# Kernel optimization log

Hardware: AMD Instinct MI355X
Metric: run time of the kernel (lower is better)

The kernel has to match this reference:

```python
import jax, jax.numpy as jnp
import numpy as np

N = 100000
F_IN = 256
F_HID = 256
F_OUT = 40
E = 3200000


def setup_inputs() -> dict:
    key = jax.random.key(0)
    ks = jax.random.split(key, 8)
    x = jax.random.normal(ks[0], (N, F_IN), dtype=jnp.float32)
    edge_index = jax.random.randint(ks[1], (2, E), 0, N, dtype=jnp.int64)
    s1 = 1.0 / np.sqrt(F_IN)
    s2 = 1.0 / np.sqrt(F_HID)
    W1 = jax.random.uniform(ks[2], (F_IN, F_HID), jnp.float32, -s1, s1)
    b1 = jnp.zeros((F_HID,), jnp.float32)
    W2 = jax.random.uniform(ks[3], (F_HID, F_HID), jnp.float32, -s2, s2)
    b2 = jnp.zeros((F_HID,), jnp.float32)
    Wlin = jax.random.uniform(ks[4], (F_HID, F_OUT), jnp.float32, -s2, s2)
    blin = jax.random.uniform(ks[5], (F_OUT,), jnp.float32, -s2, s2)
    return {"x": x, "edge_index": edge_index, "W1": W1, "b1": b1,
            "W2": W2, "b2": b2, "Wlin": Wlin, "blin": blin}


def _gcn_conv(x, src, dst, deg_inv_sqrt, W, b):
    # PyG GCNConv: linear transform, then sym-normalized aggregation, then bias
    h = x @ W                                    # [N, F]
    coef = deg_inv_sqrt[src] * deg_inv_sqrt[dst]  # [E+N]
    msgs = h[src] * coef[:, None]                # gather + scale
    agg = jax.ops.segment_sum(msgs, dst, num_segments=x.shape[0])
    return agg + b


def reference(x, edge_index, W1, b1, W2, b2, Wlin, blin):
    n = x.shape[0]
    # add self-loops (static shape: E + N)
    loops = jnp.arange(n, dtype=edge_index.dtype)
    src = jnp.concatenate([edge_index[0], loops])
    dst = jnp.concatenate([edge_index[1], loops])
    deg = jax.ops.segment_sum(jnp.ones_like(dst, dtype=x.dtype), dst, num_segments=n)
    deg_inv_sqrt = jnp.where(deg > 0, jax.lax.rsqrt(deg), 0.0)
    # dropout is identity in eval mode (training=False)
    h = _gcn_conv(x, src, dst, deg_inv_sqrt, W1, b1)
    h = _gcn_conv(h, src, dst, deg_inv_sqrt, W2, b2)
    logits = h @ Wlin + blin
    return jax.nn.log_softmax(logits, axis=1)
```

## Files before the change

kernel.cpp:

```cpp
#include <hip/hip_runtime.h>
#include <hip/hip_bf16.h>

#define FDIM 256
#define FOUT 40
#define RPB 256

typedef __attribute__((ext_vector_type(8))) short short8;
typedef __attribute__((ext_vector_type(4))) float floatx4;

__device__ __forceinline__ float bf2f(unsigned short u) {
  unsigned int x = ((unsigned int)u) << 16;
  float f;
  __builtin_memcpy(&f, &x, 4);
  return f;
}
__device__ __forceinline__ unsigned short f2bf(float f) {
  __hip_bfloat16 h = __float2bfloat16(f);
  unsigned short u;
  __builtin_memcpy(&u, &h, 2);
  return u;
}
__device__ __forceinline__ float blo(unsigned int v) {
  unsigned int x = v << 16; float f; __builtin_memcpy(&f, &x, 4); return f;
}
__device__ __forceinline__ float bhi(unsigned int v) {
  unsigned int x = v & 0xFFFF0000u; float f; __builtin_memcpy(&f, &x, 4); return f;
}


__global__ void detect_k(const int* __restrict__ raw, int nwords, int* __restrict__ flag) {
  if (threadIdx.x == 0) *flag = 0;
  __syncthreads();
  int found = 0;
  for (int w = 1 + 2 * threadIdx.x; w < nwords; w += 512)
    if (raw[w] != 0) { found = 1; break; }
  if (found) atomicOr(flag, 1);
}

__global__ void normalize_k(const int* __restrict__ raw, const int* __restrict__ flag,
                            int* __restrict__ srcN, int* __restrict__ dstN, int e) {
  int i = blockIdx.x * 256 + threadIdx.x;
  if (i >= e) return;
  if (*flag) {
    srcN[i] = raw[i];
    dstN[i] = raw[e + i];
  } else {
    srcN[i] = raw[2 * i];
    dstN[i] = raw[2 * (e + i)];
  }
}


__global__ void zero_cnt_k(int* cnt, int n) {
  int i = blockIdx.x * 256 + threadIdx.x;
  if (i < n) cnt[i] = 0;
}

__global__ void count_k(const int* __restrict__ dst, int* __restrict__ cnt, int e, int n) {
  int i = blockIdx.x * 256 + threadIdx.x;
  if (i < e) {
    int d = dst[i];
    if (d >= 0 && d < n) atomicAdd(&cnt[d], 1);
  }
}

__global__ void dis_leg_k(const int* __restrict__ cnt, float* __restrict__ dis, int n) {
  int i = blockIdx.x * 256 + threadIdx.x;
  if (i < n) dis[i] = rsqrtf((float)cnt[i] + 1.0f);
}

__global__ void scan_a_k(const int* __restrict__ cnt, int* __restrict__ excl,
                         int* __restrict__ bsum, int n) {
  __shared__ int sh[1024];
  int t = threadIdx.x;
  int gid = blockIdx.x * 1024 + t;
  int v = (gid < n) ? cnt[gid] : 0;
  sh[t] = v;
  __syncthreads();
  for (int off = 1; off < 1024; off <<= 1) {
    int x = (t >= off) ? sh[t - off] : 0;
    __syncthreads();
    sh[t] += x;
    __syncthreads();
  }
  if (gid < n) excl[gid] = sh[t] - v;
  if (t == 1023) bsum[blockIdx.x] = sh[1023];
}

__global__ void scan_b_k(int* __restrict__ bsum, int nb) {
  __shared__ int sh[1024];
  int t = threadIdx.x;
  int v = (t < nb) ? bsum[t] : 0;
  sh[t] = v;
  __syncthreads();
  for (int off = 1; off < 1024; off <<= 1) {
    int x = (t >= off) ? sh[t - off] : 0;
    __syncthreads();
    sh[t] += x;
    __syncthreads();
  }
  if (t < nb) bsum[t] = sh[t] - v;
}

__global__ void scan_c_k(int* __restrict__ row_ptr, const int* __restrict__ bsum,
                         const int* __restrict__ cnt, int* __restrict__ cursor, int n) {
  int gid = blockIdx.x * 1024 + threadIdx.x;
  if (gid < n) {
    int r = row_ptr[gid] + bsum[blockIdx.x];
    row_ptr[gid] = r;
    cursor[gid] = r;
    if (gid == n - 1) row_ptr[n] = r + cnt[gid];
  }
}

__global__ void fill_k(const int* __restrict__ src, const int* __restrict__ dst,
                       int* __restrict__ cursor, int* __restrict__ col, int e, int n) {
  int i = blockIdx.x * 256 + threadIdx.x;
  if (i < e) {
    int d = dst[i];
    if (d >= 0 && d < n) {
      int slot = atomicAdd(&cursor[d], 1);
      int s = src[i];
      s = min(max(s, 0), n - 1);
      col[slot] = s;
    }
  }
}


__global__ __launch_bounds__(512) void zerob_k(int* __restrict__ bcnt, int nbuck) {
  int t = threadIdx.x;
  if (t < nbuck) bcnt[t] = 0;
}

__global__ __launch_bounds__(256) void bhist_k(
    const int* __restrict__ raw, const int* __restrict__ flag,
    int* __restrict__ bcnt, int e, int n, int nbuck, int cpb) {
  __shared__ int hist[512];
  int t = threadIdx.x;
  for (int b = t; b < nbuck; b += 256) hist[b] = 0;
  __syncthreads();
  int fl = *flag;
  int start = blockIdx.x * cpb;
  int endc = min(e, start + cpb);
  for (int i = start + t; i < endc; i += 256) {
    int d = fl ? raw[e + i] : raw[2 * (e + i)];
    if (d >= 0 && d < n) atomicAdd(&hist[d >> 8], 1);
  }
  __syncthreads();
  for (int b = t; b < nbuck; b += 256)
    if (hist[b]) atomicAdd(&bcnt[b], hist[b]);
}

__global__ __launch_bounds__(512) void bscan_k(
    const int* __restrict__ bcnt, int* __restrict__ bbase,
    int* __restrict__ bcur, int nbuck) {
  __shared__ int sh[512];
  int t = threadIdx.x;
  int v = (t < nbuck) ? bcnt[t] : 0;
  sh[t] = v;
  __syncthreads();
  for (int off = 1; off < 512; off <<= 1) {
    int x = (t >= off) ? sh[t - off] : 0;
    __syncthreads();
    sh[t] += x;
    __syncthreads();
  }
  if (t < nbuck) {
    int ex = sh[t] - v;
    bbase[t] = ex;
    bcur[t] = ex;
  }
  if (t == nbuck - 1) bbase[nbuck] = sh[t];
}

__global__ __launch_bounds__(1024) void bin2_k(
    const int* __restrict__ raw, const int* __restrict__ flag,
    int* __restrict__ bcur, unsigned int* __restrict__ binned,
    int e, int n, int nbuck, int cpb) {
  __shared__ int hist[512];
  __shared__ int base_[512];
  __shared__ int cnt2[512];
  int t = threadIdx.x;
  int fl = *flag;
  int start = blockIdx.x * cpb;
  int endc = min(e, start + cpb);
  for (int b = t; b < nbuck; b += 1024) { hist[b] = 0; cnt2[b] = 0; }
  __syncthreads();
  for (int i = start + t; i < endc; i += 1024) {
    int d = fl ? raw[e + i] : raw[2 * (e + i)];
    if (d >= 0 && d < n) atomicAdd(&hist[d >> 8], 1);
  }
  __syncthreads();
  for (int b = t; b < nbuck; b += 1024) {
    int h = hist[b];
    base_[b] = h ? atomicAdd(&bcur[b], h) : 0;
  }
  __syncthreads();
  for (int i = start + t; i < endc; i += 1024) {
    int d = fl ? raw[e + i] : raw[2 * (e + i)];
    if (d >= 0 && d < n) {
      int s = fl ? raw[i] : raw[2 * i];
      s = min(max(s, 0), n - 1);
      int bk = d >> 8;
      int pos = base_[bk] + atomicAdd(&cnt2[bk], 1);
      binned[pos] = (((unsigned int)(d & 255)) << 17) | (unsigned int)s;
    }
  }
}

__global__ __launch_bounds__(256) void scatcnt_k(
    const unsigned int* __restrict__ binned, const int* __restrict__ bbase,
    int* __restrict__ row_ptr, float* __restrict__ dis,
    int* __restrict__ col, int n) {
  __shared__ int cnt[RPB];
  __shared__ int sc[RPB];
  __shared__ int cur[RPB];
  int b = blockIdx.x;
  int r0 = b * RPB;
  int r1 = min(n, r0 + RPB);
  int nr = r1 - r0;
  int t = threadIdx.x;
  cnt[t] = 0;
  __syncthreads();
  int e0 = bbase[b], e1 = bbase[b + 1];
  for (int i = e0 + t; i < e1; i += 256)
    atomicAdd(&cnt[binned[i] >> 17], 1);
  __syncthreads();
  int v = cnt[t];
  if (t < nr) dis[r0 + t] = rsqrtf((float)v + 1.0f);
  sc[t] = v;
  __syncthreads();
  for (int off = 1; off < 256; off <<= 1) {
    int x = (t >= off) ? sc[t - off] : 0;
    __syncthreads();
    sc[t] += x;
    __syncthreads();
  }
  int base = e0 + sc[t] - v;
  cur[t] = base;
  if (t < nr) row_ptr[r0 + t] = base;
  if (t == 0 && r1 == n) row_ptr[n] = e1;
  __syncthreads();
  for (int i = e0 + t; i < e1; i += 256) {
    unsigned int p = binned[i];
    int dlow = (int)(p >> 17);
    int slot = atomicAdd(&cur[dlow], 1);
    col[slot] = (int)(p & 0x1FFFF);
  }
}


__global__ __launch_bounds__(64) void wc_k(const float* __restrict__ W2,
                                           const float* __restrict__ Wlin,
                                           float* __restrict__ Wc) {
  __shared__ float row[FDIM];
  int k = blockIdx.x, t = threadIdx.x;
  for (int j = t; j < FDIM; j += 64) row[j] = W2[(size_t)k * FDIM + j];
  __syncthreads();
  if (t < FOUT) {
    float acc = 0.f;
    for (int j = 0; j < FDIM; ++j) acc += row[j] * Wlin[(size_t)j * FOUT + t];
    Wc[(size_t)k * FOUT + t] = acc;
  }
}

__global__ __launch_bounds__(64) void wfull_k(const float* __restrict__ W1,
                                              const float* __restrict__ Wc,
                                              float* __restrict__ Wfull) {
  __shared__ float row[FDIM];
  int k = blockIdx.x, t = threadIdx.x;
  for (int j = t; j < FDIM; j += 64) row[j] = W1[(size_t)k * FDIM + j];
  __syncthreads();
  if (t < FOUT) {
    float acc = 0.f;
    for (int j = 0; j < FDIM; ++j) acc += row[j] * Wc[(size_t)j * FOUT + t];
    Wfull[(size_t)k * FOUT + t] = acc;
  }
}

__global__ __launch_bounds__(64) void rvec_k(const float* __restrict__ b1,
                                             const float* __restrict__ Wc,
                                             const float* __restrict__ b2,
                                             const float* __restrict__ Wlin,
                                             const float* __restrict__ blin,
                                             float* __restrict__ b1c,
                                             float* __restrict__ r2) {
  int t = threadIdx.x;
  if (t < FOUT) {
    float a = 0.f, b = blin[t];
    for (int j = 0; j < FDIM; ++j) {
      a += b1[j] * Wc[(size_t)j * FOUT + t];
      b += b2[j] * Wlin[(size_t)j * FOUT + t];
    }
    b1c[t] = a;
    r2[t] = b;
  }
}

__global__ void wft_k(const float* __restrict__ Wfull, unsigned short* __restrict__ WfT) {
  int o = blockIdx.x, k = threadIdx.x;
  WfT[(size_t)o * FDIM + k] = (o < FOUT) ? f2bf(Wfull[(size_t)k * FOUT + o]) : (unsigned short)0;
}


__global__ __launch_bounds__(256) void proj_k(
    const float* __restrict__ X, const unsigned short* __restrict__ WfT,
    const float* __restrict__ dis, unsigned int* __restrict__ Ys32, int M) {
  __shared__ __align__(16) unsigned short Asm[64 * 40];
  __shared__ __align__(16) unsigned short Bsm[48 * 264];
  int t = threadIdx.x;
  int block_m = blockIdx.x * 64;
  int lane = t & 63, wave = t >> 6;
  int q = lane >> 4, rcol = lane & 15;
  for (int idx = t; idx < 48 * 256; idx += 256) {
    int o = idx >> 8, k = idx & 255;
    Bsm[o * 264 + k] = WfT[(size_t)o * FDIM + k];
  }
  floatx4 acc[3] = {};
  int arow = t >> 2, cc = (t & 3) * 8;
  int gm = block_m + arow;
  for (int kk = 0; kk < FDIM; kk += 32) {
    __syncthreads();
    {
      float4 v0 = {0, 0, 0, 0}, v1 = {0, 0, 0, 0};
      if (gm < M) {
        v0 = *(const float4*)(X + (size_t)gm * FDIM + kk + cc);
        v1 = *(const float4*)(X + (size_t)gm * FDIM + kk + cc + 4);
      }
      short8 pk;
      pk[0] = (short)f2bf(v0.x); pk[1] = (short)f2bf(v0.y);
      pk[2] = (short)f2bf(v0.z); pk[3] = (short)f2bf(v0.w);
      pk[4] = (short)f2bf(v1.x); pk[5] = (short)f2bf(v1.y);
      pk[6] = (short)f2bf(v1.z); pk[7] = (short)f2bf(v1.w);
      *(short8*)(Asm + arow * 40 + cc) = pk;
    }
    __syncthreads();
    short8 af = *(const short8*)(Asm + (wave * 16 + rcol) * 40 + q * 8);
    short8 b0 = *(const short8*)(Bsm + (rcol)*264 + kk + q * 8);
    short8 b1f = *(const short8*)(Bsm + (16 + rcol) * 264 + kk + q * 8);
    short8 b2f = *(const short8*)(Bsm + (32 + rcol) * 264 + kk + q * 8);
    acc[0] = __builtin_amdgcn_mfma_f32_16x16x32_bf16(af, b0, acc[0], 0, 0, 0);
    acc[1] = __builtin_amdgcn_mfma_f32_16x16x32_bf16(af, b1f, acc[1], 0, 0, 0);
    acc[2] = __builtin_amdgcn_mfma_f32_16x16x32_bf16(af, b2f, acc[2], 0, 0, 0);
  }
  __syncthreads();
#pragma unroll
  for (int rr = 0; rr < 4; ++rr) {
    int ml = wave * 16 + q * 4 + rr;
    int m = block_m + ml;
    float sc = (m < M) ? dis[m] : 0.f;
    unsigned short* lrow = Asm + ml * 40;
    lrow[rcol] = f2bf(acc[0][rr] * sc);
    lrow[16 + rcol] = f2bf(acc[1][rr] * sc);
    if (rcol < 8) lrow[32 + rcol] = f2bf(acc[2][rr] * sc);
  }
  __syncthreads();
  const unsigned int* A32 = (const unsigned int*)Asm;
  for (int idx = t; idx < 64 * 20; idx += 256) {
    int r = idx / 20, c = idx - r * 20;
    int m = block_m + r;
    if (m < M) Ys32[(size_t)m * 20 + c] = A32[idx];
  }
}


__global__ __launch_bounds__(256) void agg1_k(
    const unsigned int* __restrict__ T32, const int* __restrict__ row_ptr,
    const int* __restrict__ col, const float* __restrict__ dis,
    const float* __restrict__ b1c, unsigned int* __restrict__ O32, int n) {
  int wave = threadIdx.x >> 6, lane = threadIdx.x & 63;
  int wid = blockIdx.x * 4 + wave;
  int nw = gridDim.x * 4;
  int e = lane / 20;
  int fp = lane - e * 20;
  if (e > 2) { e = 2; fp = 19; }
  bool e0 = (e == 0), e1 = (e == 1);
  bool g0 = e0;
  float2 bv = ((const float2*)b1c)[fp];
  for (int i = wid; i < n; i += nw) {
    unsigned int sv = T32[(size_t)i * 20 + fp];
    float a0 = g0 ? blo(sv) : 0.f;
    float a1 = g0 ? bhi(sv) : 0.f;
    int beg = row_ptr[i], end = row_ptr[i + 1];
    for (int j0 = beg; j0 < end; j0 += 64) {
      int jj = j0 + lane;
      int cs = (jj < end) ? col[jj] : 0;
      int cc = min(64, end - j0);
      int kf = cc - cc % 24;
      int k = 0;
      for (; k < kf; k += 24) {
        int sel[8];
#pragma unroll
        for (int u = 0; u < 8; ++u) {
          int sa = __builtin_amdgcn_readlane(cs, k + 3 * u);
          int sb = __builtin_amdgcn_readlane(cs, k + 3 * u + 1);
          int sc2 = __builtin_amdgcn_readlane(cs, k + 3 * u + 2);
          sel[u] = e0 ? sa : (e1 ? sb : sc2);
        }
        unsigned int g[8];
#pragma unroll
        for (int u = 0; u < 8; ++u) g[u] = T32[(size_t)sel[u] * 20 + fp];
#pragma unroll
        for (int u = 0; u < 8; ++u) { a0 += blo(g[u]); a1 += bhi(g[u]); }
      }
      if (k < cc) {
        int sel[8];
        float w[8];
#pragma unroll
        for (int u = 0; u < 8; ++u) {
          int kb = k + 3 * u;
          int sa = __builtin_amdgcn_readlane(cs, kb & 63);
          int sb = __builtin_amdgcn_readlane(cs, (kb + 1) & 63);
          int sc2 = __builtin_amdgcn_readlane(cs, (kb + 2) & 63);
          sel[u] = e0 ? sa : (e1 ? sb : sc2);
          w[u] = (kb + e < cc) ? 1.f : 0.f;
        }
        unsigned int g[8];
#pragma unroll
        for (int u = 0; u < 8; ++u) g[u] = T32[(size_t)sel[u] * 20 + fp];
#pragma unroll
        for (int u = 0; u < 8; ++u) {
          a0 = fmaf(w[u], blo(g[u]), a0);
          a1 = fmaf(w[u], bhi(g[u]), a1);
        }
      }
    }
    a0 += __shfl(a0, fp + 20) + __shfl(a0, fp + 40);
    a1 += __shfl(a1, fp + 20) + __shfl(a1, fp + 40);
    if (g0) {
      float di = dis[i];
      unsigned int p = (unsigned int)f2bf((di * a0 + bv.x) * di) |
                       ((unsigned int)f2bf((di * a1 + bv.y) * di) << 16);
      O32[(size_t)i * 20 + fp] = p;
    }
  }
}

__global__ __launch_bounds__(256) void agg2_k(
    const unsigned int* __restrict__ T32, const int* __restrict__ row_ptr,
    const int* __restrict__ col, const float* __restrict__ dis,
    const float* __restrict__ r2, float* __restrict__ out, int n) {
  int wave = threadIdx.x >> 6, lane = threadIdx.x & 63;
  int wid = blockIdx.x * 4 + wave;
  int nw = gridDim.x * 4;
  int e = lane / 20;
  int fp = lane - e * 20;
  if (e > 2) { e = 2; fp = 19; }
  bool e0 = (e == 0), e1 = (e == 1);
  bool g0 = e0;
  float2 rv = ((const float2*)r2)[fp];
  for (int i = wid; i < n; i += nw) {
    unsigned int sv = T32[(size_t)i * 20 + fp];
    float a0 = g0 ? blo(sv) : 0.f;
    float a1 = g0 ? bhi(sv) : 0.f;
    int beg = row_ptr[i], end = row_ptr[i + 1];
    for (int j0 = beg; j0 < end; j0 += 64) {
      int jj = j0 + lane;
      int cs = (jj < end) ? col[jj] : 0;
      int cc = min(64, end - j0);
      int kf = cc - cc % 24;
      int k = 0;
      for (; k < kf; k += 24) {
        int sel[8];
#pragma unroll
        for (int u = 0; u < 8; ++u) {
          int sa = __builtin_amdgcn_readlane(cs, k + 3 * u);
          int sb = __builtin_amdgcn_readlane(cs, k + 3 * u + 1);
          int sc2 = __builtin_amdgcn_readlane(cs, k + 3 * u + 2);
          sel[u] = e0 ? sa : (e1 ? sb : sc2);
        }
        unsigned int g[8];
#pragma unroll
        for (int u = 0; u < 8; ++u) g[u] = T32[(size_t)sel[u] * 20 + fp];
#pragma unroll
        for (int u = 0; u < 8; ++u) { a0 += blo(g[u]); a1 += bhi(g[u]); }
      }
      if (k < cc) {
        int sel[8];
        float w[8];
#pragma unroll
        for (int u = 0; u < 8; ++u) {
          int kb = k + 3 * u;
          int sa = __builtin_amdgcn_readlane(cs, kb & 63);
          int sb = __builtin_amdgcn_readlane(cs, (kb + 1) & 63);
          int sc2 = __builtin_amdgcn_readlane(cs, (kb + 2) & 63);
          sel[u] = e0 ? sa : (e1 ? sb : sc2);
          w[u] = (kb + e < cc) ? 1.f : 0.f;
        }
        unsigned int g[8];
#pragma unroll
        for (int u = 0; u < 8; ++u) g[u] = T32[(size_t)sel[u] * 20 + fp];
#pragma unroll
        for (int u = 0; u < 8; ++u) {
          a0 = fmaf(w[u], blo(g[u]), a0);
          a1 = fmaf(w[u], bhi(g[u]), a1);
        }
      }
    }
    a0 += __shfl(a0, fp + 20) + __shfl(a0, fp + 40);
    a1 += __shfl(a1, fp + 20) + __shfl(a1, fp + 40);
    float di = dis[i];
    float v0 = g0 ? (di * a0 + rv.x) : -3.4e38f;
    float v1 = g0 ? (di * a1 + rv.y) : -3.4e38f;
    float m = fmaxf(v0, v1);
#pragma unroll
    for (int off = 32; off; off >>= 1) m = fmaxf(m, __shfl_xor(m, off));
    float s = g0 ? (__expf(v0 - m) + __expf(v1 - m)) : 0.f;
#pragma unroll
    for (int off = 32; off; off >>= 1) s += __shfl_xor(s, off);
    float lg = m + __logf(s);
    if (g0) {
      float2 o = {v0 - lg, v1 - lg};
      *(float2*)(out + (size_t)i * FOUT + 2 * fp) = o;
    }
  }
}


extern "C" void kernel_launch(void* const* d_in, const int* in_sizes, int n_in,
                              void* d_out, int out_size, void* d_ws, size_t ws_size,
                              hipStream_t stream) {
  const float* x   = (const float*)d_in[0];
  const int* eraw  = (const int*)d_in[1];
  const float* W1  = (const float*)d_in[2];
  const float* b1  = (const float*)d_in[3];
  const float* W2  = (const float*)d_in[4];
  const float* b2  = (const float*)d_in[5];
  const float* Wl  = (const float*)d_in[6];
  const float* bl  = (const float*)d_in[7];
  float* out = (float*)d_out;

  const int N = in_sizes[0] / FDIM;
  const int E = in_sizes[1] / 2;

  char* w = (char*)d_ws;
  size_t off = 0;
  auto take = [&](size_t bytes) {
    void* p = w + off;
    off = (off + bytes + 255) & ~(size_t)255;
    return p;
  };
  int* cnt     = (int*)take((size_t)N * 4);
  int* cursor  = (int*)take((size_t)N * 4);
  int* row_ptr = (int*)take((size_t)(N + 1) * 4);
  float* dis   = (float*)take((size_t)N * 4);
  int* bsum    = (int*)take(4096);
  int* eflag   = (int*)take(256);
  int* bcnt    = (int*)take(512 * 4);
  int* bbase   = (int*)take(513 * 4);
  int* bcur    = (int*)take(512 * 4);
  float* Wc    = (float*)take((size_t)FDIM * FOUT * 4);
  float* Wfull = (float*)take((size_t)FDIM * FOUT * 4);
  unsigned short* WfT = (unsigned short*)take((size_t)48 * FDIM * 2);
  float* b1c   = (float*)take(256);
  float* r2    = (float*)take(256);
  int* colx    = (int*)take((size_t)E * 4);

  size_t pairBytes = (size_t)2 * E * 4;
  size_t tabBytes  = (size_t)N * FOUT * 2;
  size_t rABytes = pairBytes > tabBytes ? pairBytes : tabBytes;
  char* regionA = (char*)take(rABytes);
  int* srcN = (int*)regionA;
  int* dstN = srcN + E;
  unsigned int* Ys32 = (unsigned int*)regionA;
  size_t binBytes = (size_t)E * 4;
  size_t rBBytes = binBytes > tabBytes ? binBytes : tabBytes;
  char* regionB = (char*)take(rBBytes);
  unsigned int* binned = (unsigned int*)regionB;
  unsigned int* Z1s32 = (unsigned int*)regionB;
  (void)n_in; (void)out_size; (void)ws_size;

  int gE = (E + 255) / 256;
  int gN = (N + 255) / 256;
  int NB = (N + 1023) / 1024;
  int gP = (N + 63) / 64;
  int nbuck = (N + RPB - 1) / RPB;
  bool bucketed = (N <= (1 << 17));

  int probe_words = 65536 < 2 * E ? 65536 : 2 * E;
  hipLaunchKernelGGL(detect_k, dim3(1), dim3(256), 0, stream, eraw, probe_words, eflag);

  if (bucketed) {
    int nblk = 256;
    int cpb = (E + nblk - 1) / nblk;
    hipLaunchKernelGGL(zerob_k, dim3(1), dim3(512), 0, stream, bcnt, nbuck);
    hipLaunchKernelGGL(bhist_k, dim3(nblk), dim3(256), 0, stream,
                       eraw, eflag, bcnt, E, N, nbuck, cpb);
    hipLaunchKernelGGL(bscan_k, dim3(1), dim3(512), 0, stream, bcnt, bbase, bcur, nbuck);
    hipLaunchKernelGGL(bin2_k, dim3(nblk), dim3(1024), 0, stream,
                       eraw, eflag, bcur, binned, E, N, nbuck, cpb);
    hipLaunchKernelGGL(scatcnt_k, dim3(nbuck), dim3(256), 0, stream,
                       binned, bbase, row_ptr, dis, colx, N);
  } else {
    hipLaunchKernelGGL(normalize_k, dim3(gE), dim3(256), 0, stream, eraw, eflag, srcN, dstN, E);
    hipLaunchKernelGGL(zero_cnt_k, dim3(gN), dim3(256), 0, stream, cnt, N);
    hipLaunchKernelGGL(count_k, dim3(gE), dim3(256), 0, stream, dstN, cnt, E, N);
    hipLaunchKernelGGL(dis_leg_k, dim3(gN), dim3(256), 0, stream, cnt, dis, N);
    hipLaunchKernelGGL(scan_a_k, dim3(NB), dim3(1024), 0, stream, cnt, row_ptr, bsum, N);
    hipLaunchKernelGGL(scan_b_k, dim3(1), dim3(1024), 0, stream, bsum, NB);
    hipLaunchKernelGGL(scan_c_k, dim3(NB), dim3(1024), 0, stream, row_ptr, bsum, cnt, cursor, N);
    hipLaunchKernelGGL(fill_k, dim3(gE), dim3(256), 0, stream, srcN, dstN, cursor, colx, E, N);
  }

  hipLaunchKernelGGL(wc_k, dim3(FDIM), dim3(64), 0, stream, W2, Wl, Wc);
  hipLaunchKernelGGL(wfull_k, dim3(FDIM), dim3(64), 0, stream, W1, Wc, Wfull);
  hipLaunchKernelGGL(rvec_k, dim3(1), dim3(64), 0, stream, b1, Wc, b2, Wl, bl, b1c, r2);
  hipLaunchKernelGGL(wft_k, dim3(48), dim3(FDIM), 0, stream, Wfull, WfT);

  hipLaunchKernelGGL(proj_k, dim3(gP), dim3(256), 0, stream, x, WfT, dis, Ys32, N);
  hipLaunchKernelGGL(agg1_k, dim3(2048), dim3(256), 0, stream,
                     Ys32, row_ptr, colx, dis, b1c, Z1s32, N);
  hipLaunchKernelGGL(agg2_k, dim3(2048), dim3(256), 0, stream,
                     Z1s32, row_ptr, colx, dis, r2, out, N);
}
```

Before: 463.8 us.

## Gather 8-byte features per lane with 6 edges per wave in aggregation

The aggregation kernels now give each lane 4 bf16 features (8-byte loads) and spread 6 edges across a wave's 60 active lanes, instead of 2 features and 3 edges. Source indices are stored pre-multiplied by the 80-byte row stride, and ds_bpermute replaces the readlane-and-select sequence for handing out indices. The goal is fewer, wider gather instructions and less scalar index work per edge. In exchange, 4 lanes sit idle, the cross-lane reduction gets longer, and col values can overflow int if n*80 grows beyond 2^31.

```diff
diff --git a/kernel.cpp b/kernel.cpp
--- a/kernel.cpp
+++ b/kernel.cpp
@@ -4,6 +4,7 @@
 #define FDIM 256
 #define FOUT 40
 #define RPB 256
+#define ROWB 80
 
 typedef __attribute__((ext_vector_type(8))) short short8;
 typedef __attribute__((ext_vector_type(4))) float floatx4;
@@ -122,7 +123,7 @@
       int slot = atomicAdd(&cursor[d], 1);
       int s = src[i];
       s = min(max(s, 0), n - 1);
-      col[slot] = s;
+      col[slot] = s * ROWB;
     }
   }
 }
@@ -246,7 +247,7 @@
     unsigned int p = binned[i];
     int dlow = (int)(p >> 17);
     int slot = atomicAdd(&cur[dlow], 1);
-    col[slot] = (int)(p & 0x1FFFF);
+    col[slot] = (int)(p & 0x1FFFF) * ROWB;
   }
 }
 
@@ -372,67 +373,64 @@
   int wave = threadIdx.x >> 6, lane = threadIdx.x & 63;
   int wid = blockIdx.x * 4 + wave;
   int nw = gridDim.x * 4;
-  int e = lane / 20;
-  int fp = lane - e * 20;
-  if (e > 2) { e = 2; fp = 19; }
-  bool e0 = (e == 0), e1 = (e == 1);
-  bool g0 = e0;
-  float2 bv = ((const float2*)b1c)[fp];
+  int e = lane / 10;
+  int fp2 = lane - e * 10;
+  if (e > 5) { e = 5; fp2 = 0; }
+  int e4 = e * 4;
+  bool g0 = (e == 0);
+  float4 bv = *(const float4*)(b1c + 4 * fp2);
+  const char* Tb = (const char*)T32 + fp2 * 8;
   for (int i = wid; i < n; i += nw) {
-    unsigned int sv = T32[(size_t)i * 20 + fp];
-    float a0 = g0 ? blo(sv) : 0.f;
-    float a1 = g0 ? bhi(sv) : 0.f;
+    uint2 sv = *(const uint2*)(Tb + (size_t)i * ROWB);
+    float a0 = g0 ? blo(sv.x) : 0.f;
+    float a1 = g0 ? bhi(sv.x) : 0.f;
+    float a2 = g0 ? blo(sv.y) : 0.f;
+    float a3 = g0 ? bhi(sv.y) : 0.f;
     int beg = row_ptr[i], end = row_ptr[i + 1];
     for (int j0 = beg; j0 < end; j0 += 64) {
       int jj = j0 + lane;
       int cs = (jj < end) ? col[jj] : 0;
       int cc = min(64, end - j0);
-      int kf = cc - cc % 24;
       int k = 0;
-      for (; k < kf; k += 24) {
-        int sel[8];
-#pragma unroll
-        for (int u = 0; u < 8; ++u) {
-          int sa = __builtin_amdgcn_readlane(cs, k + 3 * u);
-          int sb = __builtin_amdgcn_readlane(cs, k + 3 * u + 1);
-          int sc2 = __builtin_amdgcn_readlane(cs, k + 3 * u + 2);
-          sel[u] = e0 ? sa : (e1 ? sb : sc2);
-        }
-        unsigned int g[8];
-#pragma unroll
-        for (int u = 0; u < 8; ++u) g[u] = T32[(size_t)sel[u] * 20 + fp];
-#pragma unroll
-        for (int u = 0; u < 8; ++u) { a0 += blo(g[u]); a1 += bhi(g[u]); }
-      }
-      if (k < cc) {
-        int sel[8];
-        float w[8];
-#pragma unroll
-        for (int u = 0; u < 8; ++u) {
-          int kb = k + 3 * u;
-          int sa = __builtin_amdgcn_readlane(cs, kb & 63);
-          int sb = __builtin_amdgcn_readlane(cs, (kb + 1) & 63);
-          int sc2 = __builtin_amdgcn_readlane(cs, (kb + 2) & 63);
-          sel[u] = e0 ? sa : (e1 ? sb : sc2);
-          w[u] = (kb + e < cc) ? 1.f : 0.f;
-        }
-        unsigned int g[8];
-#pragma unroll
-        for (int u = 0; u < 8; ++u) g[u] = T32[(size_t)sel[u] * 20 + fp];
-#pragma unroll
-        for (int u = 0; u < 8; ++u) {
-          a0 = fmaf(w[u], blo(g[u]), a0);
-          a1 = fmaf(w[u], bhi(g[u]), a1);
+      for (; k + 24 <= cc; k += 24) {
+        int off[4];
+#pragma unroll
+        for (int u = 0; u < 4; ++u)
+          off[u] = __builtin_amdgcn_ds_bpermute((k + 6 * u) * 4 + e4, cs);
+        uint2 g[4];
+#pragma unroll
+        for (int u = 0; u < 4; ++u)
+          g[u] = *(const uint2*)(Tb + (unsigned int)off[u]);
+#pragma unroll
+        for (int u = 0; u < 4; ++u) {
+          a0 += blo(g[u].x); a1 += bhi(g[u].x);
+          a2 += blo(g[u].y); a3 += bhi(g[u].y);
         }
       }
-    }
-    a0 += __shfl(a0, fp + 20) + __shfl(a0, fp + 40);
-    a1 += __shfl(a1, fp + 20) + __shfl(a1, fp + 40);
+      for (; k < cc; k += 6) {
+        int off = __builtin_amdgcn_ds_bpermute(k * 4 + e4, cs);
+        float wgt = (k + e < cc) ? 1.f : 0.f;
+        uint2 g = *(const uint2*)(Tb + (unsigned int)off);
+        a0 = fmaf(wgt, blo(g.x), a0);
+        a1 = fmaf(wgt, bhi(g.x), a1);
+        a2 = fmaf(wgt, blo(g.y), a2);
+        a3 = fmaf(wgt, bhi(g.y), a3);
+      }
+    }
+    a0 += __shfl(a0, lane + 30); a1 += __shfl(a1, lane + 30);
+    a2 += __shfl(a2, lane + 30); a3 += __shfl(a3, lane + 30);
+    a0 += __shfl(a0, lane + 10) + __shfl(a0, lane + 20);
+    a1 += __shfl(a1, lane + 10) + __shfl(a1, lane + 20);
+    a2 += __shfl(a2, lane + 10) + __shfl(a2, lane + 20);
+    a3 += __shfl(a3, lane + 10) + __shfl(a3, lane + 20);
     if (g0) {
       float di = dis[i];
-      unsigned int p = (unsigned int)f2bf((di * a0 + bv.x) * di) |
-                       ((unsigned int)f2bf((di * a1 + bv.y) * di) << 16);
-      O32[(size_t)i * 20 + fp] = p;
+      uint2 p;
+      p.x = (unsigned int)f2bf((di * a0 + bv.x) * di) |
+            ((unsigned int)f2bf((di * a1 + bv.y) * di) << 16);
+      p.y = (unsigned int)f2bf((di * a2 + bv.z) * di) |
+            ((unsigned int)f2bf((di * a3 + bv.w) * di) << 16);
+      *(uint2*)((char*)O32 + (size_t)i * ROWB + fp2 * 8) = p;
     }
   }
 }
@@ -444,75 +442,71 @@
   int wave = threadIdx.x >> 6, lane = threadIdx.x & 63;
   int wid = blockIdx.x * 4 + wave;
   int nw = gridDim.x * 4;
-  int e = lane / 20;
-  int fp = lane - e * 20;
-  if (e > 2) { e = 2; fp = 19; }
-  bool e0 = (e == 0), e1 = (e == 1);
-  bool g0 = e0;
-  float2 rv = ((const float2*)r2)[fp];
+  int e = lane / 10;
+  int fp2 = lane - e * 10;
+  if (e > 5) { e = 5; fp2 = 0; }
+  int e4 = e * 4;
+  bool g0 = (e == 0);
+  float4 rv = *(const float4*)(r2 + 4 * fp2);
+  const char* Tb = (const char*)T32 + fp2 * 8;
   for (int i = wid; i < n; i += nw) {
-    unsigned int sv = T32[(size_t)i * 20 + fp];
-    float a0 = g0 ? blo(sv) : 0.f;
-    float a1 = g0 ? bhi(sv) : 0.f;
+    uint2 sv = *(const uint2*)(Tb + (size_t)i * ROWB);
+    float a0 = g0 ? blo(sv.x) : 0.f;
+    float a1 = g0 ? bhi(sv.x) : 0.f;
+    float a2 = g0 ? blo(sv.y) : 0.f;
+    float a3 = g0 ? bhi(sv.y) : 0.f;
     int beg = row_ptr[i], end = row_ptr[i + 1];
     for (int j0 = beg; j0 < end; j0 += 64) {
       int jj = j0 + lane;
       int cs = (jj < end) ? col[jj] : 0;
       int cc = min(64, end - j0);
-      int kf = cc - cc % 24;
       int k = 0;
-      for (; k < kf; k += 24) {
-        int sel[8];
-#pragma unroll
-        for (int u = 0; u < 8; ++u) {
-          int sa = __builtin_amdgcn_readlane(cs, k + 3 * u);
-          int sb = __builtin_amdgcn_readlane(cs, k + 3 * u + 1);
-          int sc2 = __builtin_amdgcn_readlane(cs, k + 3 * u + 2);
-          sel[u] = e0 ? sa : (e1 ? sb : sc2);
-        }
-        unsigned int g[8];
-#pragma unroll
-        for (int u = 0; u < 8; ++u) g[u] = T32[(size_t)sel[u] * 20 + fp];
-#pragma unroll
-        for (int u = 0; u < 8; ++u) { a0 += blo(g[u]); a1 += bhi(g[u]); }
-      }
-      if (k < cc) {
-        int sel[8];
-        float w[8];
-#pragma unroll
-        for (int u = 0; u < 8; ++u) {
-          int kb = k + 3 * u;
-          int sa = __builtin_amdgcn_readlane(cs, kb & 63);
-          int sb = __builtin_amdgcn_readlane(cs, (kb + 1) & 63);
-          int sc2 = __builtin_amdgcn_readlane(cs, (kb + 2) & 63);
-          sel[u] = e0 ? sa : (e1 ? sb : sc2);
-          w[u] = (kb + e < cc) ? 1.f : 0.f;
-        }
-        unsigned int g[8];
-#pragma unroll
-        for (int u = 0; u < 8; ++u) g[u] = T32[(size_t)sel[u] * 20 + fp];
-#pragma unroll
-        for (int u = 0; u < 8; ++u) {
-          a0 = fmaf(w[u], blo(g[u]), a0);
-          a1 = fmaf(w[u], bhi(g[u]), a1);
+      for (; k + 24 <= cc; k += 24) {
+        int off[4];
+#pragma unroll
+        for (int u = 0; u < 4; ++u)
+          off[u] = __builtin_amdgcn_ds_bpermute((k + 6 * u) * 4 + e4, cs);
+        uint2 g[4];
+#pragma unroll
+        for (int u = 0; u < 4; ++u)
+          g[u] = *(const uint2*)(Tb + (unsigned int)off[u]);
+#pragma unroll
+        for (int u = 0; u < 4; ++u) {
+          a0 += blo(g[u].x); a1 += bhi(g[u].x);
+          a2 += blo(g[u].y); a3 += bhi(g[u].y);
         }
       }
-    }
-    a0 += __shfl(a0, fp + 20) + __shfl(a0, fp + 40);
-    a1 += __shfl(a1, fp + 20) + __shfl(a1, fp + 40);
+      for (; k < cc; k += 6) {
+        int off = __builtin_amdgcn_ds_bpermute(k * 4 + e4, cs);
+        float wgt = (k + e < cc) ? 1.f : 0.f;
+        uint2 g = *(const uint2*)(Tb + (unsigned int)off);
+        a0 = fmaf(wgt, blo(g.x), a0);
+        a1 = fmaf(wgt, bhi(g.x), a1);
+        a2 = fmaf(wgt, blo(g.y), a2);
+        a3 = fmaf(wgt, bhi(g.y), a3);
+      }
+    }
+    a0 += __shfl(a0, lane + 30); a1 += __shfl(a1, lane + 30);
+    a2 += __shfl(a2, lane + 30); a3 += __shfl(a3, lane + 30);
+    a0 += __shfl(a0, lane + 10) + __shfl(a0, lane + 20);
+    a1 += __shfl(a1, lane + 10) + __shfl(a1, lane + 20);
+    a2 += __shfl(a2, lane + 10) + __shfl(a2, lane + 20);
+    a3 += __shfl(a3, lane + 10) + __shfl(a3, lane + 20);
     float di = dis[i];
     float v0 = g0 ? (di * a0 + rv.x) : -3.4e38f;
     float v1 = g0 ? (di * a1 + rv.y) : -3.4e38f;
-    float m = fmaxf(v0, v1);
+    float v2 = g0 ? (di * a2 + rv.z) : -3.4e38f;
+    float v3 = g0 ? (di * a3 + rv.w) : -3.4e38f;
+    float m = fmaxf(fmaxf(v0, v1), fmaxf(v2, v3));
 #pragma unroll
     for (int off = 32; off; off >>= 1) m = fmaxf(m, __shfl_xor(m, off));
-    float s = g0 ? (__expf(v0 - m) + __expf(v1 - m)) : 0.f;
+    float s = g0 ? (__expf(v0 - m) + __expf(v1 - m) + __expf(v2 - m) + __expf(v3 - m)) : 0.f;
 #pragma unroll
     for (int off = 32; off; off >>= 1) s += __shfl_xor(s, off);
     float lg = m + __logf(s);
     if (g0) {
-      float2 o = {v0 - lg, v1 - lg};
-      *(float2*)(out + (size_t)i * FOUT + 2 * fp) = o;
+      float4 o = {v0 - lg, v1 - lg, v2 - lg, v3 - lg};
+      *(float4*)(out + (size_t)i * FOUT + 4 * fp2) = o;
     }
   }
 }
```

After: 427.0 us (median of 2 runs). -7.9%, faster.
